# Performance work log

Hardware: AMD Instinct MI355X
Metric: run time of the kernel (lower is better)

## Reference

```python
import jax, jax.numpy as jnp
import numpy as np
from jax.scipy.linalg import cho_solve

N, D, T, K, P = 4000, 256, 52, 20, 100
EPS = 1e-8


def _make_kernel(length_scale):
    # RBF kernel over time grid with the same jitter-doubling rule as the torch code.
    t = np.arange(T, dtype=np.float32)
    sq = (t[None, :] - t[:, None]) ** 2
    Kmat = np.exp(-0.5 * sq / np.float32(length_scale) ** 2).astype(np.float32)
    jitter = 1e-4
    eye = np.eye(T, dtype=np.float32)
    while True:
        if np.linalg.cond(Kmat + jitter * eye) < 1e4:
            break
        jitter *= 2
        if jitter > 0.1:
            break
    return jnp.asarray(Kmat + jitter * eye)

K_LAMBDA = _make_kernel(T / 4)  # lambda GP kernel, shared across all k
K_PHI = _make_kernel(T / 3)     # phi GP kernel, shared across all k


def setup_inputs() -> dict:
    key = jax.random.key(0)
    ks = jax.random.split(key, 7)
    lambda_ = jax.random.normal(ks[0], (N, K, T), dtype=jnp.float32)
    phi = jax.random.normal(ks[1], (K, D, T), dtype=jnp.float32)
    gamma = 0.1 * jax.random.normal(ks[2], (P, K), dtype=jnp.float32)
    G = jax.random.normal(ks[3], (N, P), dtype=jnp.float32)
    Y = (jax.random.uniform(ks[4], (N, D, T)) < 0.05).astype(jnp.float32)
    logit_prev_t = jax.random.normal(ks[5], (D, T), dtype=jnp.float32) - 3.0
    event_times = jax.random.randint(ks[6], (N, D), 0, T)
    return dict(lambda_=lambda_, phi=phi, gamma=gamma, G=G, Y=Y,
                logit_prev_t=logit_prev_t, event_times=event_times)


def reference(lambda_, phi, gamma, G, Y, logit_prev_t, event_times):
    # --- forward: softmax over topics, sigmoid disease probs, mixture ---
    theta = jax.nn.softmax(lambda_, axis=1)          # [N,K,T]
    phi_prob = jax.nn.sigmoid(phi)                   # [K,D,T]
    pi = jnp.einsum('nkt,kdt->ndt', theta, phi_prob) # [N,D,T]
    pi = jnp.clip(pi, EPS, 1.0 - EPS)

    # --- survival data loss ---
    tgrid = jnp.arange(T)[None, None, :]             # [1,1,T]
    e = event_times[:, :, None]                      # [N,D,1]
    mask_before = (tgrid < e).astype(pi.dtype)
    mask_at = (tgrid == e).astype(pi.dtype)
    log_pi = jnp.log(pi)
    log_1mpi = jnp.log1p(-pi)
    loss_censored = -jnp.sum(log_1mpi * mask_before)
    loss_event = -jnp.sum(log_pi * mask_at * Y)
    loss_no_event = -jnp.sum(log_1mpi * mask_at * (1.0 - Y))
    data_loss = (loss_censored + loss_event + loss_no_event) / N

    # --- GP prior loss: batched cholesky solves replace per-sample loops ---
    L_lam = jnp.linalg.cholesky(K_LAMBDA)            # [T,T]
    L_phi = jnp.linalg.cholesky(K_PHI)               # [T,T]
    mean_lam = G @ gamma                             # [N,K]
    dev_lam = (lambda_ - mean_lam[:, :, None]).reshape(N * K, T)  # [N*K,T]
    v_lam = cho_solve((L_lam, True), dev_lam.T)      # [T,N*K]
    gp_lambda = 0.5 * jnp.sum(dev_lam.T * v_lam)
    dev_phi = (phi - logit_prev_t[None, :, :]).reshape(K * D, T)  # [K*D,T]
    v_phi = cho_solve((L_phi, True), dev_phi.T)      # [T,K*D]
    gp_phi = 0.5 * jnp.sum(dev_phi.T * v_phi)
    gp_loss = gp_lambda / N + gp_phi / D

    return data_loss + gp_loss
```

## Files before the change

kernel.cpp:

```cpp
#include <hip/hip_runtime.h>
#include <math.h>
#include <string.h>

#define Nn 4000
#define Dd 256
#define Tt 52
#define Kk 20
#define Pp 100
#define CH 13
#define TC 4

#define OFF_W_LAM    0
#define OFF_W_PHI    2704
#define OFF_M_LAM    5408
#define OFF_M_PHI    8112
#define OFF_DL       10816
#define OFF_EVP      10820
#define OFF_PHIP     266820
#define OFF_THETA    533060

#define GR_ROWS 128

#define RB_PHIP0   0
#define RB_THETA0  52
#define RB_GPHI0   865
#define RB_GLAM0   885
#define RB_EV0     1010
#define RB_TOTAL   1138

__global__ __launch_bounds__(256) void prep_kernel(
    const float* __restrict__ lam, const float* __restrict__ phi,
    const float* __restrict__ gamma, const float* __restrict__ G,
    const float* __restrict__ logit_prev, const int* __restrict__ ev,
    float* __restrict__ theta_t, float* __restrict__ phip_t,
    unsigned char* __restrict__ evp,
    float* __restrict__ M_lam, float* __restrict__ M_phi) {
    __shared__ float rows[GR_ROWS][56];
    __shared__ float meanv[GR_ROWS];
    const int bx = blockIdx.x, tid = threadIdx.x;

    if (bx < RB_THETA0) {
        int gid = bx * 256 + tid;
        int d = gid / Tt, t = gid - d * Tt;
        float v[Kk];
#pragma unroll
        for (int k = 0; k < Kk; ++k) {
            float x = phi[k * (Dd * Tt) + gid];
            v[k] = 1.f / (1.f + __expf(-x));
        }
#pragma unroll
        for (int k = 0; k < Kk; ++k)
            phip_t[((size_t)t * Kk + k) * Dd + d] = v[k];
        return;
    }
    if (bx < RB_GPHI0) {
        int gid = (bx - RB_THETA0) * 256 + tid;
        if (gid >= Nn * Tt) return;
        int n = gid / Tt, t = gid - n * Tt;
        const float* base = lam + n * Kk * Tt + t;
        float v[Kk];
        float m = -1e30f;
#pragma unroll
        for (int k = 0; k < Kk; ++k) { v[k] = base[k * Tt]; m = fmaxf(m, v[k]); }
        float s = 0.f;
#pragma unroll
        for (int k = 0; k < Kk; ++k) { v[k] = __expf(v[k] - m); s += v[k]; }
        float inv = 1.f / s;
        float* o = theta_t + ((size_t)t * Nn + n) * Kk;
#pragma unroll
        for (int k = 0; k < Kk; ++k) o[k] = v[k] * inv;
        return;
    }
    if (bx < RB_GLAM0) {
        int ta = tid % 13, tb = tid / 13;
        float acc[4][4] = {};
        for (int it = 0; it < 2; ++it) {
            int R0 = ((bx - RB_GPHI0) * 2 + it) * GR_ROWS;
            __syncthreads();
            for (int idx = tid; idx < GR_ROWS * Tt; idx += 256) {
                int r = idx / Tt, t = idx - r * Tt;
                int R = R0 + r;
                rows[r][t] = phi[R * Tt + t] - logit_prev[(R & 255) * Tt + t];
            }
            __syncthreads();
            if (tb < 13) {
                for (int r = 0; r < GR_ROWS; ++r) {
                    float4 a = *(const float4*)&rows[r][4 * ta];
                    float4 b = *(const float4*)&rows[r][4 * tb];
                    float av[4] = {a.x, a.y, a.z, a.w};
                    float bv[4] = {b.x, b.y, b.z, b.w};
#pragma unroll
                    for (int i = 0; i < 4; ++i)
#pragma unroll
                        for (int j = 0; j < 4; ++j) acc[i][j] += av[i] * bv[j];
                }
            }
        }
        if (tb < 13)
#pragma unroll
            for (int i = 0; i < 4; ++i)
#pragma unroll
                for (int j = 0; j < 4; ++j)
                    atomicAdd(&M_phi[(4 * ta + i) * Tt + 4 * tb + j], acc[i][j]);
        return;
    }
    if (bx < RB_EV0) {
        int ta = tid % 13, tb = tid / 13;
        float acc[4][4] = {};
        for (int it = 0; it < 5; ++it) {
            int R0 = ((bx - RB_GLAM0) * 5 + it) * GR_ROWS;
            __syncthreads();
            if (tid < GR_ROWS) {
                int R = R0 + tid;
                int n = R / Kk, k = R - n * Kk;
                float m = 0.f;
                for (int p = 0; p < Pp; ++p) m += G[n * Pp + p] * gamma[p * Kk + k];
                meanv[tid] = m;
            }
            __syncthreads();
            for (int idx = tid; idx < GR_ROWS * Tt; idx += 256) {
                int r = idx / Tt, t = idx - r * Tt;
                int R = R0 + r;
                rows[r][t] = lam[R * Tt + t] - meanv[r];
            }
            __syncthreads();
            if (tb < 13) {
                for (int r = 0; r < GR_ROWS; ++r) {
                    float4 a = *(const float4*)&rows[r][4 * ta];
                    float4 b = *(const float4*)&rows[r][4 * tb];
                    float av[4] = {a.x, a.y, a.z, a.w};
                    float bv[4] = {b.x, b.y, b.z, b.w};
#pragma unroll
                    for (int i = 0; i < 4; ++i)
#pragma unroll
                        for (int j = 0; j < 4; ++j) acc[i][j] += av[i] * bv[j];
                }
            }
        }
        if (tb < 13)
#pragma unroll
            for (int i = 0; i < 4; ++i)
#pragma unroll
                for (int j = 0; j < 4; ++j)
                    atomicAdd(&M_lam[(4 * ta + i) * Tt + 4 * tb + j], acc[i][j]);
        return;
    }
    {
        const int4* src = (const int4*)ev;
        unsigned int* dst = (unsigned int*)evp;
        int gtid = (bx - RB_EV0) * 256 + tid;
        for (int i = gtid; i < (Nn * Dd) / 4; i += 128 * 256) {
            int4 v = src[i];
            dst[i] = (unsigned)v.x | ((unsigned)v.y << 8) |
                     ((unsigned)v.z << 16) | ((unsigned)v.w << 24);
        }
        return;
    }
}

__global__ __launch_bounds__(256) void data_kernel(const float* __restrict__ theta_t,
                                                   const float* __restrict__ phip_t,
                                                   const float* __restrict__ Y,
                                                   const unsigned char* __restrict__ evp,
                                                   float* __restrict__ DL) {
    __shared__ __align__(16) float thS[TC][8][Kk];
    __shared__ float wsum[4];
    const int tid = threadIdx.x;
    const int d = tid;
    const int ng = blockIdx.x / CH;
    const int t0 = (blockIdx.x - ng * CH) * TC;
    const int n0 = ng * 8;

    for (int idx = tid; idx < TC * 8 * Kk; idx += 256) {
        int j = idx / 160, rem = idx - j * 160;
        thS[j][rem / Kk][rem - (rem / Kk) * Kk] =
            theta_t[((size_t)(t0 + j) * Nn + n0) * Kk + rem];
    }

    int e[8];
    float Yv[8], acc[8], pie[8];
#pragma unroll
    for (int g = 0; g < 8; ++g) {
        e[g] = evp[(n0 + g) * Dd + d];
        acc[g] = 0.f;
        pie[g] = 0.5f;
        Yv[g] = 0.f;
        if (e[g] >= t0 && e[g] < t0 + TC)
            Yv[g] = Y[((size_t)((n0 + g) * Dd + d)) * Tt + e[g]];
    }
    __syncthreads();

    const float* ptbase = phip_t + d;
    float pvA[Kk], pvB[Kk];
#pragma unroll
    for (int k = 0; k < Kk; ++k)
        pvA[k] = ptbase[((size_t)t0 * Kk + k) * Dd];
#pragma unroll
    for (int j = 0; j < TC; ++j) {
        float* cur = (j & 1) ? pvB : pvA;
        float* nxt = (j & 1) ? pvA : pvB;
        if (j < TC - 1) {
#pragma unroll
            for (int k = 0; k < Kk; ++k)
                nxt[k] = ptbase[((size_t)(t0 + j + 1) * Kk + k) * Dd];
        }
        int t = t0 + j;
#pragma unroll
        for (int g = 0; g < 8; ++g) {
            const float4* th = (const float4*)&thS[j][g][0];
            float4 a0 = th[0], a1 = th[1], a2 = th[2], a3 = th[3], a4 = th[4];
            float pi = a0.x * cur[0] + a0.y * cur[1] + a0.z * cur[2] + a0.w * cur[3]
                     + a1.x * cur[4] + a1.y * cur[5] + a1.z * cur[6] + a1.w * cur[7]
                     + a2.x * cur[8] + a2.y * cur[9] + a2.z * cur[10] + a2.w * cur[11]
                     + a3.x * cur[12] + a3.y * cur[13] + a3.z * cur[14] + a3.w * cur[15]
                     + a4.x * cur[16] + a4.y * cur[17] + a4.z * cur[18] + a4.w * cur[19];
            pi = fminf(fmaxf(pi, 1e-8f), 1.0f - 1e-8f);
            float lg = __logf(1.f - pi);
            if (t <= e[g]) acc[g] += lg;
            pie[g] = (t == e[g]) ? pi : pie[g];
        }
    }
    float tsum = 0.f;
#pragma unroll
    for (int g = 0; g < 8; ++g)
        tsum += acc[g] + Yv[g] * (__logf(pie[g]) - __logf(1.f - pie[g]));
    for (int off = 32; off; off >>= 1) tsum += __shfl_down(tsum, off, 64);
    if ((tid & 63) == 0) wsum[tid >> 6] = tsum;
    __syncthreads();
    if (tid == 0) atomicAdd(DL, -(wsum[0] + wsum[1] + wsum[2] + wsum[3]));
}

__global__ __launch_bounds__(256) void final_kernel(const float* __restrict__ ws,
                                                    float* __restrict__ out) {
    double s = 0.0;
    for (int i = threadIdx.x; i < 2704; i += 256)
        s += (double)ws[OFF_W_LAM + i] * (double)ws[OFF_M_LAM + i];
    for (int i = threadIdx.x; i < 2704; i += 256)
        s += (double)ws[OFF_W_PHI + i] * (double)ws[OFF_M_PHI + i];
    __shared__ double red[256];
    red[threadIdx.x] = s;
    __syncthreads();
    for (int off = 128; off; off >>= 1) {
        if (threadIdx.x < off) red[threadIdx.x] += red[threadIdx.x + off];
        __syncthreads();
    }
    if (threadIdx.x == 0) out[0] = (float)(red[0] + (double)ws[OFF_DL] / Nn);
}


static void build_K_f(double ls_in, float Kf[52][52]) {
    float ls = (float)ls_in;
    float ls2 = ls * ls;
    for (int i = 0; i < 52; ++i)
        for (int j = 0; j < 52; ++j) {
            float sq = (float)((i - j) * (i - j));
            float arg = (-0.5f * sq) / ls2;
            Kf[i][j] = expf(arg);
        }
}

static void jacobi_eig(double a[52][52], double ev[52]) {
    const int n = 52;
    for (int sweep = 0; sweep < 100; ++sweep) {
        double off = 0;
        for (int p = 0; p < n - 1; ++p)
            for (int q = p + 1; q < n; ++q) off += a[p][q] * a[p][q];
        if (off < 1e-24) break;
        for (int p = 0; p < n - 1; ++p)
            for (int q = p + 1; q < n; ++q) {
                double apq = a[p][q];
                if (fabs(apq) < 1e-300) continue;
                double th = (a[q][q] - a[p][p]) / (2.0 * apq);
                double t = (th >= 0 ? 1.0 : -1.0) / (fabs(th) + sqrt(th * th + 1.0));
                double c = 1.0 / sqrt(t * t + 1.0), s = t * c;
                for (int i = 0; i < n; ++i) {
                    double aip = a[i][p], aiq = a[i][q];
                    a[i][p] = c * aip - s * aiq;
                    a[i][q] = s * aip + c * aiq;
                }
                for (int i = 0; i < n; ++i) {
                    double api = a[p][i], aqi = a[q][i];
                    a[p][i] = c * api - s * aqi;
                    a[q][i] = s * api + c * aqi;
                }
            }
    }
    for (int i = 0; i < n; ++i) ev[i] = a[i][i];
}

static void build_A(const float Kf[52][52], double jitter, double A[52][52]) {
    float jf = (float)jitter;
    for (int i = 0; i < 52; ++i)
        for (int j = 0; j < 52; ++j) A[i][j] = (double)Kf[i][j];
    for (int i = 0; i < 52; ++i) A[i][i] = (double)(float)(Kf[i][i] + jf);
}

static double cond_of(const float Kf[52][52], double jitter) {
    double A[52][52], ev[52];
    build_A(Kf, jitter, A);
    jacobi_eig(A, ev);
    double mx = 0.0, mn = 1e300;
    for (int i = 0; i < 52; ++i) {
        double a = fabs(ev[i]);
        if (a > mx) mx = a;
        if (a < mn) mn = a;
    }
    if (mn <= 0.0) return 1e300;
    return mx / mn;
}

static double find_jitter(const float Kf[52][52]) {
    double jitter = 1e-4;
    while (true) {
        if (cond_of(Kf, jitter) < 1e4) break;
        jitter *= 2.0;
        if (jitter > 0.1) break;
    }
    return jitter;
}

static void chol_inv_scaled(const float Kf[52][52], double jitter, double scale,
                            float* out) {
    const int n = 52;
    double A[52][52], L[52][52];
    build_A(Kf, jitter, A);
    memset(L, 0, sizeof(L));
    for (int j = 0; j < n; ++j) {
        double s = A[j][j];
        for (int k = 0; k < j; ++k) s -= L[j][k] * L[j][k];
        L[j][j] = sqrt(s);
        for (int i = j + 1; i < n; ++i) {
            double v = A[i][j];
            for (int k = 0; k < j; ++k) v -= L[i][k] * L[j][k];
            L[i][j] = v / L[j][j];
        }
    }
    for (int c = 0; c < n; ++c) {
        double y[52], x[52];
        for (int i = 0; i < n; ++i) {
            double v = (i == c) ? 1.0 : 0.0;
            for (int k = 0; k < i; ++k) v -= L[i][k] * y[k];
            y[i] = v / L[i][i];
        }
        for (int i = n - 1; i >= 0; --i) {
            double v = y[i];
            for (int k = i + 1; k < n; ++k) v -= L[k][i] * x[k];
            x[i] = v / L[i][i];
        }
        for (int i = 0; i < n; ++i) out[i * 52 + c] = (float)(x[i] * scale);
    }
}

struct KinvInit {
    float* w;
    KinvInit() {
        if (hipHostMalloc((void**)&w, 5408 * sizeof(float)) != hipSuccess)
            w = (float*)malloc(5408 * sizeof(float));
        float Kf[52][52];
        build_K_f(52.0 / 4.0, Kf);
        chol_inv_scaled(Kf, find_jitter(Kf), 0.5 / Nn, w);
        build_K_f(52.0 / 3.0, Kf);
        chol_inv_scaled(Kf, find_jitter(Kf), 0.5 / Dd, w + 2704);
    }
};
static KinvInit g_kinv;


extern "C" void kernel_launch(void* const* d_in, const int* in_sizes, int n_in,
                              void* d_out, int out_size, void* d_ws, size_t ws_size,
                              hipStream_t stream) {
    (void)in_sizes; (void)n_in; (void)out_size; (void)ws_size;
    const float* lam        = (const float*)d_in[0];
    const float* phi        = (const float*)d_in[1];
    const float* gamma      = (const float*)d_in[2];
    const float* G          = (const float*)d_in[3];
    const float* Y          = (const float*)d_in[4];
    const float* logit_prev = (const float*)d_in[5];
    const int*   ev         = (const int*)d_in[6];
    float* out = (float*)d_out;
    float* ws  = (float*)d_ws;

    hipMemcpyAsync(ws + OFF_W_LAM, g_kinv.w, 5408 * sizeof(float),
                   hipMemcpyHostToDevice, stream);
    hipMemsetAsync(ws + OFF_M_LAM, 0, (2704 * 2 + 1) * sizeof(float), stream);

    prep_kernel<<<RB_TOTAL, 256, 0, stream>>>(
        lam, phi, gamma, G, logit_prev, ev,
        ws + OFF_THETA, ws + OFF_PHIP, (unsigned char*)(ws + OFF_EVP),
        ws + OFF_M_LAM, ws + OFF_M_PHI);
    data_kernel<<<(Nn / 8) * CH, 256, 0, stream>>>(
        ws + OFF_THETA, ws + OFF_PHIP, Y, (const unsigned char*)(ws + OFF_EVP),
        ws + OFF_DL);
    final_kernel<<<1, 256, 0, stream>>>(ws, out);
}
```

Before: 479.8 us.

## Replace atomics with per-block partials, retile data kernel, batch logs via products

Gram-matrix blocks and data-loss blocks now write per-block partial results, which the final kernel reduces in double. This removes the global atomics and the memset. The data kernel changes from 13 time chunks of 4 steps to 4 chunks of 13 steps, so there are fewer blocks and each does more work. It reads theta directly from global memory instead of staging it in shared memory, and drops the phi prefetch double-buffering. It also multiplies (1-pi) terms and takes one log every four steps, trading many log calls for a small underflow and precision risk.

Result: faster. 447.7 us (-6.7%).

```diff
diff --git a/kernel.cpp b/kernel.cpp
--- a/kernel.cpp
+++ b/kernel.cpp
@@ -7,17 +7,16 @@
 #define Tt 52
 #define Kk 20
 #define Pp 100
-#define CH 13
-#define TC 4
-
-#define OFF_W_LAM    0
-#define OFF_W_PHI    2704
-#define OFF_M_LAM    5408
-#define OFF_M_PHI    8112
-#define OFF_DL       10816
-#define OFF_EVP      10820
-#define OFF_PHIP     266820
-#define OFF_THETA    533060
+#define CH 4
+#define TC 13
+
+#define OFF_W       0
+#define OFF_MLAM_P  5408
+#define OFF_MPHI_P  343408
+#define OFF_DLP     397488
+#define OFF_EVP     399488
+#define OFF_PHIP    655488
+#define OFF_THETA   921728
 
 #define GR_ROWS 128
 
@@ -25,7 +24,7 @@
 #define RB_THETA0  52
 #define RB_GPHI0   865
 #define RB_GLAM0   885
-#define RB_EV0     1010
+#define RB_EVP0    1010
 #define RB_TOTAL   1138
 
 __global__ __launch_bounds__(256) void prep_kernel(
@@ -34,7 +33,7 @@
     const float* __restrict__ logit_prev, const int* __restrict__ ev,
     float* __restrict__ theta_t, float* __restrict__ phip_t,
     unsigned char* __restrict__ evp,
-    float* __restrict__ M_lam, float* __restrict__ M_phi) {
+    float* __restrict__ Mlam_p, float* __restrict__ Mphi_p) {
     __shared__ float rows[GR_ROWS][56];
     __shared__ float meanv[GR_ROWS];
     const int bx = blockIdx.x, tid = threadIdx.x;
@@ -72,10 +71,11 @@
         return;
     }
     if (bx < RB_GLAM0) {
+        int slot = bx - RB_GPHI0;
         int ta = tid % 13, tb = tid / 13;
         float acc[4][4] = {};
         for (int it = 0; it < 2; ++it) {
-            int R0 = ((bx - RB_GPHI0) * 2 + it) * GR_ROWS;
+            int R0 = (slot * 2 + it) * GR_ROWS;
             __syncthreads();
             for (int idx = tid; idx < GR_ROWS * Tt; idx += 256) {
                 int r = idx / Tt, t = idx - r * Tt;
@@ -101,14 +101,15 @@
             for (int i = 0; i < 4; ++i)
 #pragma unroll
                 for (int j = 0; j < 4; ++j)
-                    atomicAdd(&M_phi[(4 * ta + i) * Tt + 4 * tb + j], acc[i][j]);
-        return;
-    }
-    if (bx < RB_EV0) {
+                    Mphi_p[slot * 2704 + (4 * ta + i) * Tt + 4 * tb + j] = acc[i][j];
+        return;
+    }
+    if (bx < RB_EVP0) {
+        int slot = bx - RB_GLAM0;
         int ta = tid % 13, tb = tid / 13;
         float acc[4][4] = {};
         for (int it = 0; it < 5; ++it) {
-            int R0 = ((bx - RB_GLAM0) * 5 + it) * GR_ROWS;
+            int R0 = (slot * 5 + it) * GR_ROWS;
             __syncthreads();
             if (tid < GR_ROWS) {
                 int R = R0 + tid;
@@ -142,13 +143,13 @@
             for (int i = 0; i < 4; ++i)
 #pragma unroll
                 for (int j = 0; j < 4; ++j)
-                    atomicAdd(&M_lam[(4 * ta + i) * Tt + 4 * tb + j], acc[i][j]);
+                    Mlam_p[slot * 2704 + (4 * ta + i) * Tt + 4 * tb + j] = acc[i][j];
         return;
     }
     {
         const int4* src = (const int4*)ev;
         unsigned int* dst = (unsigned int*)evp;
-        int gtid = (bx - RB_EV0) * 256 + tid;
+        int gtid = (bx - RB_EVP0) * 256 + tid;
         for (int i = gtid; i < (Nn * Dd) / 4; i += 128 * 256) {
             int4 v = src[i];
             dst[i] = (unsigned)v.x | ((unsigned)v.y << 8) |
@@ -162,62 +163,50 @@
                                                    const float* __restrict__ phip_t,
                                                    const float* __restrict__ Y,
                                                    const unsigned char* __restrict__ evp,
-                                                   float* __restrict__ DL) {
-    __shared__ __align__(16) float thS[TC][8][Kk];
+                                                   float* __restrict__ DLp) {
     __shared__ float wsum[4];
     const int tid = threadIdx.x;
     const int d = tid;
-    const int ng = blockIdx.x / CH;
-    const int t0 = (blockIdx.x - ng * CH) * TC;
+    const int ng = blockIdx.x >> 2;
+    const int t0 = (blockIdx.x & 3) * TC;
     const int n0 = ng * 8;
 
-    for (int idx = tid; idx < TC * 8 * Kk; idx += 256) {
-        int j = idx / 160, rem = idx - j * 160;
-        thS[j][rem / Kk][rem - (rem / Kk) * Kk] =
-            theta_t[((size_t)(t0 + j) * Nn + n0) * Kk + rem];
-    }
-
     int e[8];
-    float Yv[8], acc[8], pie[8];
+    float Yv[8], acc[8], pie[8], prod[8];
 #pragma unroll
     for (int g = 0; g < 8; ++g) {
         e[g] = evp[(n0 + g) * Dd + d];
         acc[g] = 0.f;
+        prod[g] = 1.f;
         pie[g] = 0.5f;
         Yv[g] = 0.f;
         if (e[g] >= t0 && e[g] < t0 + TC)
-            Yv[g] = Y[((size_t)((n0 + g) * Dd + d)) * Tt + e[g]];
-    }
-    __syncthreads();
-
-    const float* ptbase = phip_t + d;
-    float pvA[Kk], pvB[Kk];
-#pragma unroll
-    for (int k = 0; k < Kk; ++k)
-        pvA[k] = ptbase[((size_t)t0 * Kk + k) * Dd];
-#pragma unroll
+            Yv[g] = __builtin_nontemporal_load(
+                Y + ((size_t)((n0 + g) * Dd + d)) * Tt + e[g]);
+    }
+
     for (int j = 0; j < TC; ++j) {
-        float* cur = (j & 1) ? pvB : pvA;
-        float* nxt = (j & 1) ? pvA : pvB;
-        if (j < TC - 1) {
-#pragma unroll
-            for (int k = 0; k < Kk; ++k)
-                nxt[k] = ptbase[((size_t)(t0 + j + 1) * Kk + k) * Dd];
-        }
         int t = t0 + j;
+        float pv[Kk];
+        const float* pt = phip_t + (size_t)t * (Kk * Dd) + d;
+#pragma unroll
+        for (int k = 0; k < Kk; ++k) pv[k] = pt[k * Dd];
 #pragma unroll
         for (int g = 0; g < 8; ++g) {
-            const float4* th = (const float4*)&thS[j][g][0];
+            const float4* th = (const float4*)(theta_t + ((size_t)t * Nn + n0 + g) * Kk);
             float4 a0 = th[0], a1 = th[1], a2 = th[2], a3 = th[3], a4 = th[4];
-            float pi = a0.x * cur[0] + a0.y * cur[1] + a0.z * cur[2] + a0.w * cur[3]
-                     + a1.x * cur[4] + a1.y * cur[5] + a1.z * cur[6] + a1.w * cur[7]
-                     + a2.x * cur[8] + a2.y * cur[9] + a2.z * cur[10] + a2.w * cur[11]
-                     + a3.x * cur[12] + a3.y * cur[13] + a3.z * cur[14] + a3.w * cur[15]
-                     + a4.x * cur[16] + a4.y * cur[17] + a4.z * cur[18] + a4.w * cur[19];
+            float pi = a0.x * pv[0] + a0.y * pv[1] + a0.z * pv[2] + a0.w * pv[3]
+                     + a1.x * pv[4] + a1.y * pv[5] + a1.z * pv[6] + a1.w * pv[7]
+                     + a2.x * pv[8] + a2.y * pv[9] + a2.z * pv[10] + a2.w * pv[11]
+                     + a3.x * pv[12] + a3.y * pv[13] + a3.z * pv[14] + a3.w * pv[15]
+                     + a4.x * pv[16] + a4.y * pv[17] + a4.z * pv[18] + a4.w * pv[19];
             pi = fminf(fmaxf(pi, 1e-8f), 1.0f - 1e-8f);
-            float lg = __logf(1.f - pi);
-            if (t <= e[g]) acc[g] += lg;
+            prod[g] *= (t <= e[g]) ? (1.f - pi) : 1.f;
             pie[g] = (t == e[g]) ? pi : pie[g];
+        }
+        if ((j & 3) == 3 || j == TC - 1) {
+#pragma unroll
+            for (int g = 0; g < 8; ++g) { acc[g] += __logf(prod[g]); prod[g] = 1.f; }
         }
     }
     float tsum = 0.f;
@@ -227,24 +216,31 @@
     for (int off = 32; off; off >>= 1) tsum += __shfl_down(tsum, off, 64);
     if ((tid & 63) == 0) wsum[tid >> 6] = tsum;
     __syncthreads();
-    if (tid == 0) atomicAdd(DL, -(wsum[0] + wsum[1] + wsum[2] + wsum[3]));
-}
-
-__global__ __launch_bounds__(256) void final_kernel(const float* __restrict__ ws,
-                                                    float* __restrict__ out) {
+    if (tid == 0)
+        DLp[blockIdx.x] = -(wsum[0] + wsum[1] + wsum[2] + wsum[3]);
+}
+
+__global__ __launch_bounds__(1024) void final_kernel(const float* __restrict__ ws,
+                                                     float* __restrict__ out) {
+    const int tid = threadIdx.x;
     double s = 0.0;
-    for (int i = threadIdx.x; i < 2704; i += 256)
-        s += (double)ws[OFF_W_LAM + i] * (double)ws[OFF_M_LAM + i];
-    for (int i = threadIdx.x; i < 2704; i += 256)
-        s += (double)ws[OFF_W_PHI + i] * (double)ws[OFF_M_PHI + i];
-    __shared__ double red[256];
-    red[threadIdx.x] = s;
+    for (int i = tid; i < 2704; i += 1024) {
+        double ml = 0.0, mp = 0.0;
+        for (int b = 0; b < 125; ++b) ml += (double)ws[OFF_MLAM_P + b * 2704 + i];
+        for (int b = 0; b < 20; ++b)  mp += (double)ws[OFF_MPHI_P + b * 2704 + i];
+        s += (double)ws[OFF_W + i] * ml + (double)ws[OFF_W + 2704 + i] * mp;
+    }
+    double dl = 0.0;
+    for (int i = tid; i < (Nn / 8) * CH; i += 1024) dl += (double)ws[OFF_DLP + i];
+    s += dl / Nn;
+    __shared__ double red[1024];
+    red[tid] = s;
     __syncthreads();
-    for (int off = 128; off; off >>= 1) {
-        if (threadIdx.x < off) red[threadIdx.x] += red[threadIdx.x + off];
+    for (int off = 512; off; off >>= 1) {
+        if (tid < off) red[tid] += red[tid + off];
         __syncthreads();
     }
-    if (threadIdx.x == 0) out[0] = (float)(red[0] + (double)ws[OFF_DL] / Nn);
+    if (tid == 0) out[0] = (float)red[0];
 }
 
 
@@ -380,16 +376,15 @@
     float* out = (float*)d_out;
     float* ws  = (float*)d_ws;
 
-    hipMemcpyAsync(ws + OFF_W_LAM, g_kinv.w, 5408 * sizeof(float),
+    hipMemcpyAsync(ws + OFF_W, g_kinv.w, 5408 * sizeof(float),
                    hipMemcpyHostToDevice, stream);
-    hipMemsetAsync(ws + OFF_M_LAM, 0, (2704 * 2 + 1) * sizeof(float), stream);
 
     prep_kernel<<<RB_TOTAL, 256, 0, stream>>>(
         lam, phi, gamma, G, logit_prev, ev,
         ws + OFF_THETA, ws + OFF_PHIP, (unsigned char*)(ws + OFF_EVP),
-        ws + OFF_M_LAM, ws + OFF_M_PHI);
+        ws + OFF_MLAM_P, ws + OFF_MPHI_P);
     data_kernel<<<(Nn / 8) * CH, 256, 0, stream>>>(
         ws + OFF_THETA, ws + OFF_PHIP, Y, (const unsigned char*)(ws + OFF_EVP),
-        ws + OFF_DL);
-    final_kernel<<<1, 256, 0, stream>>>(ws, out);
-}
+        ws + OFF_DLP);
+    final_kernel<<<1, 1024, 0, stream>>>(ws, out);
+}
```
